# Kernel tuning notes

Measured on AMD Instinct MI355X. Metric: run time of the kernel, lower is better.

The kernel has to match this reference:

```python
import jax, jax.numpy as jnp
import numpy as np

B, N, K, H, L = 2, 1024, 48, 128, 3
SCALE = 30.0


def _gelu(x):
    # torch.nn.GELU default is the exact erf formulation
    return jax.nn.gelu(x, approximate=False)


def _ln(x, g, b, eps=1e-5):
    mu = jnp.mean(x, axis=-1, keepdims=True)
    var = jnp.mean((x - mu) ** 2, axis=-1, keepdims=True)
    return g * (x - mu) * jax.lax.rsqrt(var + eps) + b


def _gather_nodes(nodes, idx):
    # nodes: [B,N,H], idx: [B,N,K] -> [B,N,K,H]
    b, n, k = idx.shape
    flat = idx.reshape(b, n * k)
    g = jnp.take_along_axis(nodes, flat[:, :, None], axis=1)
    return g.reshape(b, n, k, nodes.shape[-1])


def setup_inputs() -> dict:
    key = jax.random.key(0)
    ks = jax.random.split(key, 16)

    def w(k, shape, fan_in):
        return jax.random.normal(k, shape, jnp.float32) / np.sqrt(fan_in).astype(np.float32)

    kp = jax.random.split(ks[5], 9)
    inp = {
        "h_V": jax.random.normal(ks[0], (B, N, H), jnp.float32),
        "h_E": jax.random.normal(ks[1], (B, N, K, H), jnp.float32),
        "E_idx": jax.random.randint(ks[2], (B, N, K), 0, N),
        "mask_V": jnp.ones((B, N), jnp.float32),
        "mask_attend": jnp.ones((B, N, K), jnp.float32),
        # message MLP (node update): W1 [3H->H], W2, W3
        "W1": w(kp[0], (L, 3 * H, H), 3 * H), "b1": jnp.zeros((L, H), jnp.float32),
        "W2": w(kp[1], (L, H, H), H), "b2": jnp.zeros((L, H), jnp.float32),
        "W3": w(kp[2], (L, H, H), H), "b3": jnp.zeros((L, H), jnp.float32),
        # message MLP (edge update): W11 [3H->H], W12, W13
        "W11": w(kp[3], (L, 3 * H, H), 3 * H), "b11": jnp.zeros((L, H), jnp.float32),
        "W12": w(kp[4], (L, H, H), H), "b12": jnp.zeros((L, H), jnp.float32),
        "W13": w(kp[5], (L, H, H), H), "b13": jnp.zeros((L, H), jnp.float32),
        # position-wise FFN: H -> 4H -> H
        "Win": w(kp[6], (L, H, 4 * H), H), "bin_": jnp.zeros((L, 4 * H), jnp.float32),
        "Wout": w(kp[7], (L, 4 * H, H), 4 * H), "bout": jnp.zeros((L, H), jnp.float32),
        # LayerNorms
        "g1": jnp.ones((L, H), jnp.float32), "be1": jnp.zeros((L, H), jnp.float32),
        "g2": jnp.ones((L, H), jnp.float32), "be2": jnp.zeros((L, H), jnp.float32),
        "g3": jnp.ones((L, H), jnp.float32), "be3": jnp.zeros((L, H), jnp.float32),
    }
    return inp


def reference(h_V, h_E, E_idx, mask_V, mask_attend,
              W1, b1, W2, b2, W3, b3,
              W11, b11, W12, b12, W13, b13,
              Win, bin_, Wout, bout,
              g1, be1, g2, be2, g3, be3):
    # Stack of L EncLayers (eval mode, dropout = identity).
    for l in range(L):
        # --- node update: gather neighbors, concat, 3-layer MLP message ---
        hVn = _gather_nodes(h_V, E_idx)                        # [B,N,K,H]
        hVe = jnp.broadcast_to(h_V[:, :, None, :], hVn.shape)  # [B,N,K,H]
        h_EV = jnp.concatenate([hVe, h_E, hVn], axis=-1)       # [B,N,K,3H]
        m = _gelu(h_EV @ W1[l] + b1[l])
        m = _gelu(m @ W2[l] + b2[l])
        m = m @ W3[l] + b3[l]
        m = mask_attend[..., None] * m
        dh = jnp.sum(m, axis=-2) / SCALE                       # masked sum aggregate
        h_V = _ln(h_V + dh, g1[l], be1[l])
        dh = _gelu(h_V @ Win[l] + bin_[l]) @ Wout[l] + bout[l]
        h_V = _ln(h_V + dh, g2[l], be2[l])
        h_V = mask_V[..., None] * h_V
        # --- edge update ---
        hVn = _gather_nodes(h_V, E_idx)
        hVe = jnp.broadcast_to(h_V[:, :, None, :], hVn.shape)
        h_EV = jnp.concatenate([hVe, h_E, hVn], axis=-1)
        m = _gelu(h_EV @ W11[l] + b11[l])
        m = _gelu(m @ W12[l] + b12[l])
        m = m @ W13[l] + b13[l]
        h_E = _ln(h_E + m, g3[l], be3[l])
    return h_V, h_E
```

## Files before the change

kernel.cpp:

```cpp
#include <hip/hip_runtime.h>
#include <hip/hip_bf16.h>
#include <math.h>

#define BB 2
#define NN 1024
#define HH 128
#define LL 3
#define SY 136
#define SH 520
#define SX 136
#define SM 132

typedef __attribute__((ext_vector_type(8))) short s8v;
typedef __attribute__((ext_vector_type(4))) float f4v;
typedef unsigned short u16;

static __device__ __forceinline__ u16 f2bf(float x) {
  union { float f; unsigned u; } v; v.f = x;
  unsigned r = v.u + 0x7FFFu + ((v.u >> 16) & 1u);
  return (u16)(r >> 16);
}
static __device__ __forceinline__ float geluf(float x) {
  float x2 = x * x;
  float u2 = x * (1.5957691216f + 0.0713548163f * x2);
  float e = __expf(u2);
  float d = __builtin_amdgcn_rcpf(e + 1.0f);
  return x - x * d;
}

static __device__ __forceinline__ void loadB(const u16* __restrict__ Wt, int wave, int lane,
                                             s8v B0[4], s8v B1[4]) {
  const int g = lane >> 4, q = lane & 15;
  const u16* wb0 = Wt + (wave * 32 + q) * 128 + g * 8;
  const u16* wb1 = wb0 + 16 * 128;
#pragma unroll
  for (int t = 0; t < 4; ++t) { B0[t] = *(const s8v*)(wb0 + t * 32); B1[t] = *(const s8v*)(wb1 + t * 32); }
}

static __device__ __forceinline__ void gemmA(const u16* __restrict__ A,
                                             const s8v B0[4], const s8v B1[4],
                                             int lane, f4v acc[3][2]) {
  const int g = lane >> 4, q = lane & 15;
  __builtin_amdgcn_s_setprio(1);
#pragma unroll
  for (int t = 0; t < 4; ++t) {
    const u16* Ab = A + t * 32 + g * 8;
    s8v a0 = *(const s8v*)(Ab + q * SY);
    s8v a1 = *(const s8v*)(Ab + (16 + q) * SY);
    s8v a2 = *(const s8v*)(Ab + (32 + q) * SY);
    acc[0][0] = __builtin_amdgcn_mfma_f32_16x16x32_bf16(a0, B0[t], acc[0][0], 0, 0, 0);
    acc[0][1] = __builtin_amdgcn_mfma_f32_16x16x32_bf16(a0, B1[t], acc[0][1], 0, 0, 0);
    acc[1][0] = __builtin_amdgcn_mfma_f32_16x16x32_bf16(a1, B0[t], acc[1][0], 0, 0, 0);
    acc[1][1] = __builtin_amdgcn_mfma_f32_16x16x32_bf16(a1, B1[t], acc[1][1], 0, 0, 0);
    acc[2][0] = __builtin_amdgcn_mfma_f32_16x16x32_bf16(a2, B0[t], acc[2][0], 0, 0, 0);
    acc[2][1] = __builtin_amdgcn_mfma_f32_16x16x32_bf16(a2, B1[t], acc[2][1], 0, 0, 0);
  }
  __builtin_amdgcn_s_setprio(0);
}

static __device__ __forceinline__ void gemm48k128(const u16* __restrict__ A,
                                                  const u16* __restrict__ Wt,
                                                  int wave, int lane, f4v acc[3][2]) {
  const int g = lane >> 4, q = lane & 15;
  s8v B0[4], B1[4];
  const u16* wb0 = Wt + (wave * 32 + q) * 128 + g * 8;
  const u16* wb1 = wb0 + 16 * 128;
#pragma unroll
  for (int t = 0; t < 4; ++t) { B0[t] = *(const s8v*)(wb0 + t * 32); B1[t] = *(const s8v*)(wb1 + t * 32); }
#pragma unroll
  for (int t = 0; t < 4; ++t) {
    const u16* Ab = A + t * 32 + g * 8;
    s8v a0 = *(const s8v*)(Ab + q * SY);
    s8v a1 = *(const s8v*)(Ab + (16 + q) * SY);
    s8v a2 = *(const s8v*)(Ab + (32 + q) * SY);
    acc[0][0] = __builtin_amdgcn_mfma_f32_16x16x32_bf16(a0, B0[t], acc[0][0], 0, 0, 0);
    acc[0][1] = __builtin_amdgcn_mfma_f32_16x16x32_bf16(a0, B1[t], acc[0][1], 0, 0, 0);
    acc[1][0] = __builtin_amdgcn_mfma_f32_16x16x32_bf16(a1, B0[t], acc[1][0], 0, 0, 0);
    acc[1][1] = __builtin_amdgcn_mfma_f32_16x16x32_bf16(a1, B1[t], acc[1][1], 0, 0, 0);
    acc[2][0] = __builtin_amdgcn_mfma_f32_16x16x32_bf16(a2, B0[t], acc[2][0], 0, 0, 0);
    acc[2][1] = __builtin_amdgcn_mfma_f32_16x16x32_bf16(a2, B1[t], acc[2][1], 0, 0, 0);
  }
}

static __device__ __forceinline__ void zero_acc(f4v acc[3][2]) {
#pragma unroll
  for (int rt = 0; rt < 3; ++rt)
#pragma unroll
    for (int c = 0; c < 2; ++c) acc[rt][c] = (f4v){0.f, 0.f, 0.f, 0.f};
}

static __device__ __forceinline__ void store_act(const f4v acc[3][2], u16* __restrict__ Y,
                                                 int wave, int lane, const float* __restrict__ bias) {
  const int g = lane >> 4, q = lane & 15;
#pragma unroll
  for (int c = 0; c < 2; ++c) {
    const int col = wave * 32 + c * 16 + q;
    const float bv = bias[col];
#pragma unroll
    for (int rt = 0; rt < 3; ++rt)
#pragma unroll
      for (int r = 0; r < 4; ++r) {
        const int row = rt * 16 + g * 4 + r;
        Y[row * SY + col] = f2bf(geluf(acc[rt][c][r] + bv));
      }
  }
}

static __device__ __forceinline__ void stage_f32(u16* __restrict__ dst, const float* src, int tid) {
  const float4* hEr = (const float4*)src;
#pragma unroll
  for (int p = 0; p < 6; ++p) {
    int i = tid + p * 256; int row = i >> 5, c = i & 31;
    float4 v = hEr[i];
    uint2 pk;
    pk.x = (unsigned)f2bf(v.x) | ((unsigned)f2bf(v.y) << 16);
    pk.y = (unsigned)f2bf(v.z) | ((unsigned)f2bf(v.w) << 16);
    *(uint2*)(dst + row * SY + c * 4) = pk;
  }
}

static __device__ __forceinline__ void init_acc(f4v acc[3][2],
                                                const float* __restrict__ Q, const float* __restrict__ P,
                                                const int* __restrict__ eidx, int bid, int bbase,
                                                int wave, int g, int q) {
  const float* Qr = Q + (size_t)bid * 128;
  const float qv0 = Qr[wave * 32 + q];
  const float qv1 = Qr[wave * 32 + 16 + q];
#pragma unroll
  for (int rt = 0; rt < 3; ++rt)
#pragma unroll
    for (int r = 0; r < 4; ++r) {
      const int row = rt * 16 + g * 4 + r;
      const int idx = eidx[bid * 48 + row];
      const float* Pr = P + (size_t)(bbase + idx) * 128 + wave * 32;
      acc[rt][0][r] = qv0 + Pr[q];
      acc[rt][1][r] = qv1 + Pr[16 + q];
    }
}

__global__ void conv_weights(const float* __restrict__ W1, const float* __restrict__ W2,
                             const float* __restrict__ W3, const float* __restrict__ W11,
                             const float* __restrict__ W12, const float* __restrict__ W13,
                             const float* __restrict__ Win, const float* __restrict__ Wout,
                             const float* __restrict__ hV,
                             u16* __restrict__ W1bT, u16* __restrict__ W2t,
                             u16* __restrict__ W3t, u16* __restrict__ W11bT,
                             u16* __restrict__ W12t, u16* __restrict__ W13t,
                             u16* __restrict__ Wint, u16* __restrict__ Woutt,
                             u16* __restrict__ PRE, u16* __restrict__ hv0bf) {
  const int tid = blockIdx.x * blockDim.x + threadIdx.x;
  const int nt = gridDim.x * blockDim.x;
  for (int i = tid; i < LL * 128 * 128; i += nt) {
    int l = i >> 14, rem = i & 16383;
    int k = rem >> 7, n = rem & 127;
    const int o = (l * 128 + n) * 128 + k;
    const int s = l * 16384 + k * 128 + n;
    W1bT [o] = f2bf(W1 [l * 49152 + (128 + k) * 128 + n]);
    W11bT[o] = f2bf(W11[l * 49152 + (128 + k) * 128 + n]);
    W2t [o] = f2bf(W2 [s]);
    W3t [o] = f2bf(W3 [s]);
    W12t[o] = f2bf(W12[s]);
    W13t[o] = f2bf(W13[s]);
    const int ln = (l + 1 == LL) ? 0 : l + 1;
    PRE[l * 65536 + (0 * 128 + n) * 128 + k] = f2bf(W11[l * 49152 + k * 128 + n]);
    PRE[l * 65536 + (1 * 128 + n) * 128 + k] = f2bf(W11[l * 49152 + (256 + k) * 128 + n]);
    PRE[l * 65536 + (2 * 128 + n) * 128 + k] = f2bf(W1 [ln * 49152 + k * 128 + n]);
    PRE[l * 65536 + (3 * 128 + n) * 128 + k] = f2bf(W1 [ln * 49152 + (256 + k) * 128 + n]);
  }
  for (int i = tid; i < LL * 128 * 512; i += nt) {
    int l = i / (128 * 512), rem = i - l * 128 * 512;
    int k = rem / 512, u = rem - k * 512;
    Wint[(l * 512 + u) * 128 + k] = f2bf(Win[i]);
  }
  for (int i = tid; i < LL * 512 * 128; i += nt) {
    int l = i / (512 * 128), rem = i - l * 512 * 128;
    int k = rem / 128, n = rem - k * 128;
    Woutt[(l * 128 + n) * 512 + k] = f2bf(Wout[i]);
  }
  for (int i = tid; i < BB * NN * HH; i += nt) hv0bf[i] = f2bf(hV[i]);
}

__global__ __launch_bounds__(256) void pre_kernel(const u16* __restrict__ hvbf,
                                                  const u16* __restrict__ Wq,
                                                  const u16* __restrict__ Wp,
                                                  float* __restrict__ Q, float* __restrict__ P) {
  __shared__ __align__(16) u16 shX[16 * SX];
  const int tid = threadIdx.x, lane = tid & 63, wave = tid >> 6;
  const int g = lane >> 4, q = lane & 15;
  const int r0 = blockIdx.x * 16;
  { int row = tid >> 4, c = tid & 15;
    *(uint4*)(shX + row * SX + c * 8) = ((const uint4*)(hvbf + (size_t)r0 * 128))[tid]; }
  __syncthreads();
  s8v af[4];
#pragma unroll
  for (int t = 0; t < 4; ++t) af[t] = *(const s8v*)(shX + q * SX + t * 32 + g * 8);
  const u16* W = (wave < 2) ? Wq : Wp;
  float* D = (wave < 2) ? Q : P;
  const int c0 = (wave & 1) * 64;
#pragma unroll
  for (int cf = 0; cf < 4; ++cf) {
    const int col = c0 + cf * 16 + q;
    const u16* wb = W + (size_t)col * 128 + g * 8;
    f4v acc = (f4v){0.f, 0.f, 0.f, 0.f};
#pragma unroll
    for (int t = 0; t < 4; ++t)
      acc = __builtin_amdgcn_mfma_f32_16x16x32_bf16(af[t], *(const s8v*)(wb + t * 32), acc, 0, 0, 0);
#pragma unroll
    for (int r = 0; r < 4; ++r) D[(size_t)(r0 + g * 4 + r) * 128 + col] = acc[r];
  }
}

__global__ __launch_bounds__(256, 6) void node_msg(
    const float* __restrict__ hv_res, const float* __restrict__ Qn, const float* __restrict__ Pn,
    const float* hE_src, const int* __restrict__ eidx, const float* __restrict__ mask_att,
    const u16* __restrict__ W1bT, const u16* __restrict__ W2t, const u16* __restrict__ W3t,
    const float* __restrict__ b1, const float* __restrict__ b2, const float* __restrict__ b3,
    const float* __restrict__ g1, const float* __restrict__ be1,
    float* __restrict__ hv1, u16* __restrict__ hv1bf) {
  __shared__ __align__(16) u16 buf[2 * 48 * SY];
  __shared__ float sh_mask[48];
  __shared__ float sh_x[128];
  __shared__ float sh_st[2];
  u16* bufA = buf;
  u16* bufB = buf + 48 * SY;

  const int tid = threadIdx.x, lane = tid & 63, wave = tid >> 6;
  const int g = lane >> 4, q = lane & 15;
  const int bid = blockIdx.x, bbase = bid & ~(NN - 1);

  if (tid < 48) sh_mask[tid] = mask_att[bid * 48 + tid];
  f4v acc[3][2];
  init_acc(acc, Qn, Pn, eidx, bid, bbase, wave, g, q);
  stage_f32(bufA, hE_src + (size_t)bid * 6144, tid);
  s8v Ba[4], Bb[4];
  loadB(W1bT, wave, lane, Ba, Bb);
  __syncthreads();

  gemmA(bufA, Ba, Bb, lane, acc);
  loadB(W2t, wave, lane, Ba, Bb);
  store_act(acc, bufB, wave, lane, b1);
  __syncthreads();

  zero_acc(acc);
  gemmA(bufB, Ba, Bb, lane, acc);
  loadB(W3t, wave, lane, Ba, Bb);
  store_act(acc, bufA, wave, lane, b2);
  __syncthreads();

  zero_acc(acc);
  gemmA(bufA, Ba, Bb, lane, acc);

  float msum = 0.f;
#pragma unroll
  for (int k = 0; k < 48; ++k) msum += sh_mask[k];
  float p0 = 0.f, p1 = 0.f;
#pragma unroll
  for (int rt = 0; rt < 3; ++rt)
#pragma unroll
    for (int r = 0; r < 4; ++r) {
      const float mk = sh_mask[rt * 16 + g * 4 + r];
      p0 += acc[rt][0][r] * mk;
      p1 += acc[rt][1][r] * mk;
    }
  p0 += __shfl_xor(p0, 16); p0 += __shfl_xor(p0, 32);
  p1 += __shfl_xor(p1, 16); p1 += __shfl_xor(p1, 32);
  if (g == 0) {
    const int c0 = wave * 32 + q, c1 = wave * 32 + 16 + q;
    sh_x[c0] = hv_res[(size_t)bid * 128 + c0] + (p0 + b3[c0] * msum) * (1.f / 30.f);
    sh_x[c1] = hv_res[(size_t)bid * 128 + c1] + (p1 + b3[c1] * msum) * (1.f / 30.f);
  }
  __syncthreads();

  if (tid < 64) {
    float a = sh_x[tid], c2 = sh_x[tid + 64];
    float s = a + c2, ss = a * a + c2 * c2;
#pragma unroll
    for (int off = 32; off; off >>= 1) { s += __shfl_xor(s, off); ss += __shfl_xor(ss, off); }
    if (tid == 0) { float mu = s * (1.f / 128.f); sh_st[0] = mu; sh_st[1] = ss * (1.f / 128.f) - mu * mu; }
  }
  __syncthreads();
  if (tid < 128) {
    float mu = sh_st[0], rs = rsqrtf(sh_st[1] + 1e-5f);
    float v = g1[tid] * (sh_x[tid] - mu) * rs + be1[tid];
    hv1[(size_t)bid * 128 + tid] = v;
    hv1bf[(size_t)bid * 128 + tid] = f2bf(v);
  }
}

__global__ __launch_bounds__(256) void ffn_kernel(
    const float* __restrict__ hv1, const u16* __restrict__ hv1bf,
    const u16* __restrict__ Wint, const float* __restrict__ binp,
    const u16* __restrict__ Woutt, const float* __restrict__ boutp,
    const float* __restrict__ g2, const float* __restrict__ be2,
    const float* __restrict__ mask_V,
    const u16* __restrict__ PRE,
    float* __restrict__ hv2,
    float* __restrict__ Qe, float* __restrict__ Pe,
    float* __restrict__ QnN, float* __restrict__ PnN) {
  __shared__ __align__(16) u16 shX[16 * SX];
  __shared__ __align__(16) u16 shH[16 * SH];
  __shared__ float shM[8 * 128];
  const int tid = threadIdx.x, lane = tid & 63, wave = tid >> 6;
  const int g = lane >> 4, q = lane & 15;
  const int r0 = blockIdx.x * 8;

  {
    int row = tid >> 4, c = tid & 15;
    uint4 v = (uint4){0, 0, 0, 0};
    if (tid < 128) v = ((const uint4*)(hv1bf + (size_t)r0 * 128))[tid];
    *(uint4*)(shX + row * SX + c * 8) = v;
  }
  __syncthreads();

  s8v a[4];
#pragma unroll
  for (int t = 0; t < 4; ++t) a[t] = *(const s8v*)(shX + q * SX + t * 32 + g * 8);
#pragma unroll
  for (int cf = 0; cf < 8; ++cf) {
    const int u = wave * 128 + cf * 16 + q;
    const u16* wb = Wint + (size_t)u * 128 + g * 8;
    f4v acc = (f4v){0.f, 0.f, 0.f, 0.f};
#pragma unroll
    for (int t = 0; t < 4; ++t)
      acc = __builtin_amdgcn_mfma_f32_16x16x32_bf16(a[t], *(const s8v*)(wb + t * 32), acc, 0, 0, 0);
    const float bv = binp[u];
#pragma unroll
    for (int r = 0; r < 4; ++r) shH[(g * 4 + r) * SH + u] = f2bf(geluf(acc[r] + bv));
  }
  __syncthreads();

#pragma unroll
  for (int c = 0; c < 2; ++c) {
    const int col = wave * 32 + c * 16 + q;
    const u16* wb = Woutt + (size_t)col * 512 + g * 8;
    s8v Bv[16];
#pragma unroll
    for (int t = 0; t < 16; ++t) Bv[t] = *(const s8v*)(wb + t * 32);
    f4v acc = (f4v){0.f, 0.f, 0.f, 0.f};
#pragma unroll
    for (int t = 0; t < 16; ++t) {
      s8v av = *(const s8v*)(shH + q * SH + t * 32 + g * 8);
      acc = __builtin_amdgcn_mfma_f32_16x16x32_bf16(av, Bv[t], acc, 0, 0, 0);
    }
    const float bv = boutp[col];
#pragma unroll
    for (int r = 0; r < 4; ++r) {
      const int row = g * 4 + r;
      if (row < 8) shM[row * 128 + col] = acc[r] + bv;
    }
  }
  __syncthreads();

#pragma unroll
  for (int i = 0; i < 2; ++i) {
    const int row = wave * 2 + i, gr = r0 + row;
    float x0 = hv1[(size_t)gr * 128 + lane]      + shM[row * 128 + lane];
    float x1 = hv1[(size_t)gr * 128 + 64 + lane] + shM[row * 128 + 64 + lane];
    float s = x0 + x1, ss = x0 * x0 + x1 * x1;
#pragma unroll
    for (int off = 32; off; off >>= 1) { s += __shfl_xor(s, off); ss += __shfl_xor(ss, off); }
    const float mu = s * (1.f / 128.f);
    const float rs = rsqrtf(ss * (1.f / 128.f) - mu * mu + 1e-5f);
    const float mv = mask_V[gr];
    float o0 = mv * (g2[lane]      * (x0 - mu) * rs + be2[lane]);
    float o1 = mv * (g2[lane + 64] * (x1 - mu) * rs + be2[lane + 64]);
    hv2[(size_t)gr * 128 + lane] = o0;
    hv2[(size_t)gr * 128 + 64 + lane] = o1;
    shX[row * SX + lane] = f2bf(o0);
    shX[row * SX + 64 + lane] = f2bf(o1);
  }
  __syncthreads();

  s8v af[4];
#pragma unroll
  for (int t = 0; t < 4; ++t) af[t] = *(const s8v*)(shX + q * SX + t * 32 + g * 8);
  float* dst = (wave == 0) ? Qe : (wave == 1) ? Pe : (wave == 2) ? QnN : PnN;
  const u16* Wb = PRE + (size_t)(wave * 128) * 128;
#pragma unroll
  for (int cf = 0; cf < 8; ++cf) {
    const int colr = cf * 16 + q;
    const u16* wb = Wb + (size_t)colr * 128 + g * 8;
    f4v acc = (f4v){0.f, 0.f, 0.f, 0.f};
#pragma unroll
    for (int t = 0; t < 4; ++t)
      acc = __builtin_amdgcn_mfma_f32_16x16x32_bf16(af[t], *(const s8v*)(wb + t * 32), acc, 0, 0, 0);
    if (g < 2) {
#pragma unroll
      for (int r = 0; r < 4; ++r)
        dst[(size_t)(r0 + g * 4 + r) * 128 + colr] = acc[r];
    }
  }
}

__global__ __launch_bounds__(256, 5) void edge_kernel(
    const float* __restrict__ Qe, const float* __restrict__ Pe,
    const float* hE_src, const int* __restrict__ eidx,
    const u16* __restrict__ W11bT, const u16* __restrict__ W12t, const u16* __restrict__ W13t,
    const float* __restrict__ b11, const float* __restrict__ b12, const float* __restrict__ b13,
    const float* __restrict__ g3, const float* __restrict__ be3,
    float* hE_out) {
  __shared__ __align__(16) u16 buf[2 * 48 * SY];
  __shared__ float2 sh_stats[48 * 4];
  __shared__ float2 sh_statsF[48];
  __shared__ int sh_idx[48];
  u16* bufA = buf;
  u16* bufB = buf + 48 * SY;

  const int tid = threadIdx.x, lane = tid & 63, wave = tid >> 6;
  const int g = lane >> 4, q = lane & 15;
  const int bid = blockIdx.x, bbase = bid & ~(NN - 1);

  if (tid < 48) sh_idx[tid] = eidx[bid * 48 + tid];
  stage_f32(bufA, hE_src + (size_t)bid * 6144, tid);
  const float* heb = hE_src + (size_t)bid * 6144;
  float xh[3][2][4];
#pragma unroll
  for (int rt = 0; rt < 3; ++rt)
#pragma unroll
    for (int c = 0; c < 2; ++c)
#pragma unroll
      for (int r = 0; r < 4; ++r)
        xh[rt][c][r] = heb[(rt * 16 + g * 4 + r) * 128 + wave * 32 + c * 16 + q];
  __syncthreads();

  f4v acc[3][2];
  {
    const float* Qr = Qe + (size_t)bid * 128;
#pragma unroll
    for (int c = 0; c < 2; ++c) {
      const int col = wave * 32 + c * 16 + q;
      const float qv = Qr[col];
#pragma unroll
      for (int rt = 0; rt < 3; ++rt)
#pragma unroll
        for (int r = 0; r < 4; ++r) {
          const int row = rt * 16 + g * 4 + r;
          acc[rt][c][r] = qv + Pe[(size_t)(bbase + sh_idx[row]) * 128 + col];
        }
    }
  }
  gemm48k128(bufA, W11bT, wave, lane, acc);
  store_act(acc, bufB, wave, lane, b11);
  __syncthreads();

  zero_acc(acc);
  gemm48k128(bufB, W12t, wave, lane, acc);
  store_act(acc, bufA, wave, lane, b12);
  __syncthreads();

  zero_acc(acc);
  gemm48k128(bufA, W13t, wave, lane, acc);
  const float bv0 = b13[wave * 32 + q], bv1 = b13[wave * 32 + 16 + q];
#pragma unroll
  for (int rt = 0; rt < 3; ++rt)
#pragma unroll
    for (int r = 0; r < 4; ++r) {
      xh[rt][0][r] += acc[rt][0][r] + bv0;
      xh[rt][1][r] += acc[rt][1][r] + bv1;
    }

#pragma unroll
  for (int rt = 0; rt < 3; ++rt)
#pragma unroll
    for (int r = 0; r < 4; ++r) {
      float s = xh[rt][0][r] + xh[rt][1][r];
      float ss = xh[rt][0][r] * xh[rt][0][r] + xh[rt][1][r] * xh[rt][1][r];
#pragma unroll
      for (int off = 1; off < 16; off <<= 1) { s += __shfl_xor(s, off); ss += __shfl_xor(ss, off); }
      if (q == 0) sh_stats[(rt * 16 + g * 4 + r) * 4 + wave] = make_float2(s, ss);
    }
  __syncthreads();
  if (tid < 48) {
    float s = 0.f, ss = 0.f;
#pragma unroll
    for (int w = 0; w < 4; ++w) { float2 v = sh_stats[tid * 4 + w]; s += v.x; ss += v.y; }
    float mu = s * (1.f / 128.f);
    float rs = rsqrtf(ss * (1.f / 128.f) - mu * mu + 1e-5f);
    sh_statsF[tid] = make_float2(mu, rs);
  }
  __syncthreads();

  float* shOut = (float*)buf;
  const float g30 = g3[wave * 32 + q], g31 = g3[wave * 32 + 16 + q];
  const float be30 = be3[wave * 32 + q], be31 = be3[wave * 32 + 16 + q];
#pragma unroll
  for (int rt = 0; rt < 3; ++rt)
#pragma unroll
    for (int r = 0; r < 4; ++r) {
      const int row = rt * 16 + g * 4 + r;
      const float2 mf = sh_statsF[row];
      shOut[row * SM + wave * 32 + q]      = g30 * (xh[rt][0][r] - mf.x) * mf.y + be30;
      shOut[row * SM + wave * 32 + 16 + q] = g31 * (xh[rt][1][r] - mf.x) * mf.y + be31;
    }
  __syncthreads();

  float4* wdst = (float4*)(hE_out + (size_t)bid * 6144);
#pragma unroll
  for (int p = 0; p < 6; ++p) {
    const int i = tid + p * 256;
    const int row = i >> 5, c4 = i & 31;
    wdst[i] = *(const float4*)(shOut + row * SM + 4 * c4);
  }
}

extern "C" void kernel_launch(void* const* d_in, const int* in_sizes, int n_in,
                              void* d_out, int out_size, void* d_ws, size_t ws_size,
                              hipStream_t stream) {
  const float* h_V      = (const float*)d_in[0];
  const float* h_E      = (const float*)d_in[1];
  const int*   E_idx    = (const int*)d_in[2];
  const float* mask_V   = (const float*)d_in[3];
  const float* mask_att = (const float*)d_in[4];
  const float* W1   = (const float*)d_in[5];   const float* b1   = (const float*)d_in[6];
  const float* W2   = (const float*)d_in[7];   const float* b2   = (const float*)d_in[8];
  const float* W3   = (const float*)d_in[9];   const float* b3   = (const float*)d_in[10];
  const float* W11  = (const float*)d_in[11];  const float* b11  = (const float*)d_in[12];
  const float* W12  = (const float*)d_in[13];  const float* b12  = (const float*)d_in[14];
  const float* W13  = (const float*)d_in[15];  const float* b13  = (const float*)d_in[16];
  const float* Win  = (const float*)d_in[17];  const float* binp = (const float*)d_in[18];
  const float* Wout = (const float*)d_in[19];  const float* boutp= (const float*)d_in[20];
  const float* g1   = (const float*)d_in[21];  const float* be1  = (const float*)d_in[22];
  const float* g2   = (const float*)d_in[23];  const float* be2  = (const float*)d_in[24];
  const float* g3   = (const float*)d_in[25];  const float* be3  = (const float*)d_in[26];

  float* outV = (float*)d_out;
  float* outE = outV + (size_t)BB * NN * HH;

  u16* ws     = (u16*)d_ws;
  u16* W1bT   = ws;
  u16* W11bT  = W1bT  + 3 * 16384;
  u16* W2t    = W11bT + 3 * 16384;
  u16* W3t    = W2t   + 3 * 16384;
  u16* W12t   = W3t   + 3 * 16384;
  u16* W13t   = W12t  + 3 * 16384;
  u16* Wint   = W13t  + 3 * 16384;
  u16* Woutt  = Wint  + 3 * 65536;
  u16* PREb   = Woutt + 3 * 65536;
  u16* hv0bf  = PREb  + 3 * 65536;
  u16* Pbf    = hv0bf + BB * NN * HH;
  float* Pf   = (float*)(Pbf + BB * NN * HH);
  float* Qf   = Pf  + BB * NN * HH;
  float* Qn   = Qf  + BB * NN * HH;
  float* Pn   = Qn  + BB * NN * HH;
  float* Qe   = Pn  + BB * NN * HH;
  float* Pe   = Qe  + BB * NN * HH;

  conv_weights<<<512, 256, 0, stream>>>(W1, W2, W3, W11, W12, W13, Win, Wout, h_V,
                                        W1bT, W2t, W3t, W11bT, W12t, W13t, Wint, Woutt,
                                        PREb, hv0bf);

  pre_kernel<<<(BB * NN) / 16, 256, 0, stream>>>(
      hv0bf, PREb + 2 * 65536 + 2 * 16384, PREb + 2 * 65536 + 3 * 16384, Qn, Pn);

  for (int l = 0; l < LL; ++l) {
    const float* hv_res  = (l == 0) ? h_V : Qf;
    const float* hE_src  = (l == 0) ? h_E : outE;
    float*       hv2_dst = (l == 2) ? outV : Qf;

    node_msg<<<BB * NN, 256, 0, stream>>>(
        hv_res, Qn, Pn, hE_src, E_idx, mask_att,
        W1bT + l * 16384, W2t + l * 16384, W3t + l * 16384,
        b1 + l * 128, b2 + l * 128, b3 + l * 128,
        g1 + l * 128, be1 + l * 128,
        Pf, Pbf);

    ffn_kernel<<<(BB * NN) / 8, 256, 0, stream>>>(
        Pf, Pbf,
        Wint + l * 65536, binp + l * 512,
        Woutt + l * 65536, boutp + l * 128,
        g2 + l * 128, be2 + l * 128, mask_V,
        PREb + l * 65536,
        hv2_dst, Qe, Pe, Qn, Pn);

    edge_kernel<<<BB * NN, 256, 0, stream>>>(
        Qe, Pe, hE_src, E_idx,
        W11bT + l * 16384, W12t + l * 16384, W13t + l * 16384,
        b11 + l * 128, b12 + l * 128, b13 + l * 128,
        g3 + l * 128, be3 + l * 128,
        outE);
  }
}
```

Before: 317.9 us.

## Fuse layer-l edge update with layer-(l+1) node message kernel

Adds a fused kernel that runs the edge MLP and LayerNorm for layer l, then reuses the normalized h_E rows held in registers to run the node-message MLP and aggregation for layer l+1. This avoids re-reading h_E from global memory and saves one launch per layer boundary. The launch schedule is rearranged to match. The hE residual load in edge_kernel is also moved later to shorten register live ranges. The fused kernel carries more registers and more serial work per block, which may lower occupancy.

```diff
diff --git a/kernel.cpp b/kernel.cpp
--- a/kernel.cpp
+++ b/kernel.cpp
@@ -412,15 +412,6 @@
 
   if (tid < 48) sh_idx[tid] = eidx[bid * 48 + tid];
   stage_f32(bufA, hE_src + (size_t)bid * 6144, tid);
-  const float* heb = hE_src + (size_t)bid * 6144;
-  float xh[3][2][4];
-#pragma unroll
-  for (int rt = 0; rt < 3; ++rt)
-#pragma unroll
-    for (int c = 0; c < 2; ++c)
-#pragma unroll
-      for (int r = 0; r < 4; ++r)
-        xh[rt][c][r] = heb[(rt * 16 + g * 4 + r) * 128 + wave * 32 + c * 16 + q];
   __syncthreads();
 
   f4v acc[3][2];
@@ -448,6 +439,15 @@
   store_act(acc, bufA, wave, lane, b12);
   __syncthreads();
 
+  const float* heb = hE_src + (size_t)bid * 6144;
+  float xh[3][2][4];
+#pragma unroll
+  for (int rt = 0; rt < 3; ++rt)
+#pragma unroll
+    for (int c = 0; c < 2; ++c)
+#pragma unroll
+      for (int r = 0; r < 4; ++r)
+        xh[rt][c][r] = heb[(rt * 16 + g * 4 + r) * 128 + wave * 32 + c * 16 + q];
   zero_acc(acc);
   gemm48k128(bufA, W13t, wave, lane, acc);
   const float bv0 = b13[wave * 32 + q], bv1 = b13[wave * 32 + 16 + q];
@@ -500,6 +500,193 @@
     const int i = tid + p * 256;
     const int row = i >> 5, c4 = i & 31;
     wdst[i] = *(const float4*)(shOut + row * SM + 4 * c4);
+  }
+}
+
+__global__ __launch_bounds__(256, 5) void fused_edge_node(
+    const float* __restrict__ Qe, const float* __restrict__ Pe,
+    const float* hE_src, const int* __restrict__ eidx,
+    const u16* __restrict__ W11bT, const u16* __restrict__ W12t, const u16* __restrict__ W13t,
+    const float* __restrict__ b11, const float* __restrict__ b12, const float* __restrict__ b13,
+    const float* __restrict__ g3, const float* __restrict__ be3,
+    float* hE_out,
+    const float* __restrict__ hv_res, const float* __restrict__ Qn, const float* __restrict__ Pn,
+    const float* __restrict__ mask_att,
+    const u16* __restrict__ W1bT, const u16* __restrict__ W2t, const u16* __restrict__ W3t,
+    const float* __restrict__ b1, const float* __restrict__ b2, const float* __restrict__ b3,
+    const float* __restrict__ g1, const float* __restrict__ be1,
+    float* __restrict__ hv1, u16* __restrict__ hv1bf) {
+  __shared__ __align__(16) u16 buf[2 * 48 * SY];
+  __shared__ float2 sh_stats[48 * 4];
+  __shared__ float2 sh_statsF[48];
+  __shared__ int sh_idx[48];
+  __shared__ float sh_mask[48];
+  __shared__ float sh_x[128];
+  __shared__ float sh_st[2];
+  u16* bufA = buf;
+  u16* bufB = buf + 48 * SY;
+
+  const int tid = threadIdx.x, lane = tid & 63, wave = tid >> 6;
+  const int g = lane >> 4, q = lane & 15;
+  const int bid = blockIdx.x, bbase = bid & ~(NN - 1);
+
+  if (tid < 48) { sh_idx[tid] = eidx[bid * 48 + tid]; sh_mask[tid] = mask_att[bid * 48 + tid]; }
+  stage_f32(bufA, hE_src + (size_t)bid * 6144, tid);
+  __syncthreads();
+
+  f4v acc[3][2];
+  {
+    const float* Qr = Qe + (size_t)bid * 128;
+#pragma unroll
+    for (int c = 0; c < 2; ++c) {
+      const int col = wave * 32 + c * 16 + q;
+      const float qv = Qr[col];
+#pragma unroll
+      for (int rt = 0; rt < 3; ++rt)
+#pragma unroll
+        for (int r = 0; r < 4; ++r) {
+          const int row = rt * 16 + g * 4 + r;
+          acc[rt][c][r] = qv + Pe[(size_t)(bbase + sh_idx[row]) * 128 + col];
+        }
+    }
+  }
+  gemm48k128(bufA, W11bT, wave, lane, acc);
+  store_act(acc, bufB, wave, lane, b11);
+  __syncthreads();
+
+  zero_acc(acc);
+  gemm48k128(bufB, W12t, wave, lane, acc);
+  store_act(acc, bufA, wave, lane, b12);
+  __syncthreads();
+
+  const float* heb = hE_src + (size_t)bid * 6144;
+  float xh[3][2][4];
+#pragma unroll
+  for (int rt = 0; rt < 3; ++rt)
+#pragma unroll
+    for (int c = 0; c < 2; ++c)
+#pragma unroll
+      for (int r = 0; r < 4; ++r)
+        xh[rt][c][r] = heb[(rt * 16 + g * 4 + r) * 128 + wave * 32 + c * 16 + q];
+  zero_acc(acc);
+  gemm48k128(bufA, W13t, wave, lane, acc);
+  const float bv0 = b13[wave * 32 + q], bv1 = b13[wave * 32 + 16 + q];
+#pragma unroll
+  for (int rt = 0; rt < 3; ++rt)
+#pragma unroll
+    for (int r = 0; r < 4; ++r) {
+      xh[rt][0][r] += acc[rt][0][r] + bv0;
+      xh[rt][1][r] += acc[rt][1][r] + bv1;
+    }
+
+#pragma unroll
+  for (int rt = 0; rt < 3; ++rt)
+#pragma unroll
+    for (int r = 0; r < 4; ++r) {
+      float s = xh[rt][0][r] + xh[rt][1][r];
+      float ss = xh[rt][0][r] * xh[rt][0][r] + xh[rt][1][r] * xh[rt][1][r];
+#pragma unroll
+      for (int off = 1; off < 16; off <<= 1) { s += __shfl_xor(s, off); ss += __shfl_xor(ss, off); }
+      if (q == 0) sh_stats[(rt * 16 + g * 4 + r) * 4 + wave] = make_float2(s, ss);
+    }
+  __syncthreads();
+  if (tid < 48) {
+    float s = 0.f, ss = 0.f;
+#pragma unroll
+    for (int w = 0; w < 4; ++w) { float2 v = sh_stats[tid * 4 + w]; s += v.x; ss += v.y; }
+    float mu = s * (1.f / 128.f);
+    float rs = rsqrtf(ss * (1.f / 128.f) - mu * mu + 1e-5f);
+    sh_statsF[tid] = make_float2(mu, rs);
+  }
+  __syncthreads();
+
+  float* shOut = (float*)buf;
+  const float g30 = g3[wave * 32 + q], g31 = g3[wave * 32 + 16 + q];
+  const float be30 = be3[wave * 32 + q], be31 = be3[wave * 32 + 16 + q];
+#pragma unroll
+  for (int rt = 0; rt < 3; ++rt)
+#pragma unroll
+    for (int r = 0; r < 4; ++r) {
+      const int row = rt * 16 + g * 4 + r;
+      const float2 mf = sh_statsF[row];
+      shOut[row * SM + wave * 32 + q]      = g30 * (xh[rt][0][r] - mf.x) * mf.y + be30;
+      shOut[row * SM + wave * 32 + 16 + q] = g31 * (xh[rt][1][r] - mf.x) * mf.y + be31;
+    }
+  __syncthreads();
+
+  float4* wdst = (float4*)(hE_out + (size_t)bid * 6144);
+#pragma unroll
+  for (int p = 0; p < 6; ++p) {
+    const int i = tid + p * 256;
+    const int row = i >> 5, c4 = i & 31;
+    wdst[i] = *(const float4*)(shOut + row * SM + 4 * c4);
+  }
+
+  f4v acc2[3][2];
+  init_acc(acc2, Qn, Pn, eidx, bid, bbase, wave, g, q);
+  s8v Ba[4], Bb[4];
+  loadB(W1bT, wave, lane, Ba, Bb);
+  __syncthreads();
+
+#pragma unroll
+  for (int rt = 0; rt < 3; ++rt)
+#pragma unroll
+    for (int r = 0; r < 4; ++r) {
+      const int row = rt * 16 + g * 4 + r;
+      const float2 mf = sh_statsF[row];
+      bufA[row * SY + wave * 32 + q]      = f2bf(g30 * (xh[rt][0][r] - mf.x) * mf.y + be30);
+      bufA[row * SY + wave * 32 + 16 + q] = f2bf(g31 * (xh[rt][1][r] - mf.x) * mf.y + be31);
+    }
+  __syncthreads();
+
+  gemmA(bufA, Ba, Bb, lane, acc2);
+  loadB(W2t, wave, lane, Ba, Bb);
+  store_act(acc2, bufB, wave, lane, b1);
+  __syncthreads();
+
+  zero_acc(acc2);
+  gemmA(bufB, Ba, Bb, lane, acc2);
+  loadB(W3t, wave, lane, Ba, Bb);
+  store_act(acc2, bufA, wave, lane, b2);
+  __syncthreads();
+
+  zero_acc(acc2);
+  gemmA(bufA, Ba, Bb, lane, acc2);
+
+  float msum = 0.f;
+#pragma unroll
+  for (int k = 0; k < 48; ++k) msum += sh_mask[k];
+  float p0 = 0.f, p1 = 0.f;
+#pragma unroll
+  for (int rt = 0; rt < 3; ++rt)
+#pragma unroll
+    for (int r = 0; r < 4; ++r) {
+      const float mk = sh_mask[rt * 16 + g * 4 + r];
+      p0 += acc2[rt][0][r] * mk;
+      p1 += acc2[rt][1][r] * mk;
+    }
+  p0 += __shfl_xor(p0, 16); p0 += __shfl_xor(p0, 32);
+  p1 += __shfl_xor(p1, 16); p1 += __shfl_xor(p1, 32);
+  if (g == 0) {
+    const int c0 = wave * 32 + q, c1 = wave * 32 + 16 + q;
+    sh_x[c0] = hv_res[(size_t)bid * 128 + c0] + (p0 + b3[c0] * msum) * (1.f / 30.f);
+    sh_x[c1] = hv_res[(size_t)bid * 128 + c1] + (p1 + b3[c1] * msum) * (1.f / 30.f);
+  }
+  __syncthreads();
+
+  if (tid < 64) {
+    float a = sh_x[tid], c2 = sh_x[tid + 64];
+    float s = a + c2, ss = a * a + c2 * c2;
+#pragma unroll
+    for (int off = 32; off; off >>= 1) { s += __shfl_xor(s, off); ss += __shfl_xor(ss, off); }
+    if (tid == 0) { float mu = s * (1.f / 128.f); sh_st[0] = mu; sh_st[1] = ss * (1.f / 128.f) - mu * mu; }
+  }
+  __syncthreads();
+  if (tid < 128) {
+    float mu = sh_st[0], rs = rsqrtf(sh_st[1] + 1e-5f);
+    float v = g1[tid] * (sh_x[tid] - mu) * rs + be1[tid];
+    hv1[(size_t)bid * 128 + tid] = v;
+    hv1bf[(size_t)bid * 128 + tid] = f2bf(v);
   }
 }
 
@@ -552,31 +739,41 @@
   pre_kernel<<<(BB * NN) / 16, 256, 0, stream>>>(
       hv0bf, PREb + 2 * 65536 + 2 * 16384, PREb + 2 * 65536 + 3 * 16384, Qn, Pn);
 
-  for (int l = 0; l < LL; ++l) {
-    const float* hv_res  = (l == 0) ? h_V : Qf;
-    const float* hE_src  = (l == 0) ? h_E : outE;
-    float*       hv2_dst = (l == 2) ? outV : Qf;
-
-    node_msg<<<BB * NN, 256, 0, stream>>>(
-        hv_res, Qn, Pn, hE_src, E_idx, mask_att,
-        W1bT + l * 16384, W2t + l * 16384, W3t + l * 16384,
-        b1 + l * 128, b2 + l * 128, b3 + l * 128,
-        g1 + l * 128, be1 + l * 128,
-        Pf, Pbf);
-
-    ffn_kernel<<<(BB * NN) / 8, 256, 0, stream>>>(
-        Pf, Pbf,
-        Wint + l * 65536, binp + l * 512,
-        Woutt + l * 65536, boutp + l * 128,
-        g2 + l * 128, be2 + l * 128, mask_V,
-        PREb + l * 65536,
-        hv2_dst, Qe, Pe, Qn, Pn);
-
-    edge_kernel<<<BB * NN, 256, 0, stream>>>(
-        Qe, Pe, hE_src, E_idx,
+  node_msg<<<BB * NN, 256, 0, stream>>>(
+      h_V, Qn, Pn, h_E, E_idx, mask_att,
+      W1bT, W2t, W3t, b1, b2, b3, g1, be1, Pf, Pbf);
+  ffn_kernel<<<(BB * NN) / 8, 256, 0, stream>>>(
+      Pf, Pbf, Wint, binp, Woutt, boutp, g2, be2, mask_V, PREb,
+      Qf, Qe, Pe, Qn, Pn);
+
+  for (int l = 0; l < 2; ++l) {
+    const float* hE_in = (l == 0) ? h_E : outE;
+    const int lp = l + 1;
+    fused_edge_node<<<BB * NN, 256, 0, stream>>>(
+        Qe, Pe, hE_in, E_idx,
         W11bT + l * 16384, W12t + l * 16384, W13t + l * 16384,
         b11 + l * 128, b12 + l * 128, b13 + l * 128,
         g3 + l * 128, be3 + l * 128,
-        outE);
-  }
-}
+        outE,
+        Qf, Qn, Pn, mask_att,
+        W1bT + lp * 16384, W2t + lp * 16384, W3t + lp * 16384,
+        b1 + lp * 128, b2 + lp * 128, b3 + lp * 128,
+        g1 + lp * 128, be1 + lp * 128,
+        Pf, Pbf);
+
+    ffn_kernel<<<(BB * NN) / 8, 256, 0, stream>>>(
+        Pf, Pbf,
+        Wint + lp * 65536, binp + lp * 512,
+        Woutt + lp * 65536, boutp + lp * 128,
+        g2 + lp * 128, be2 + lp * 128, mask_V,
+        PREb + lp * 65536,
+        (lp == 2) ? outV : Qf, Qe, Pe, Qn, Pn);
+  }
+
+  edge_kernel<<<BB * NN, 256, 0, stream>>>(
+      Qe, Pe, outE, E_idx,
+      W11bT + 2 * 16384, W12t + 2 * 16384, W13t + 2 * 16384,
+      b11 + 2 * 128, b12 + 2 * 128, b13 + 2 * 128,
+      g3 + 2 * 128, be3 + 2 * 128,
+      outE);
+}
```

Result: no change. 318.4 us (+0.1%).
